# Performance work log

Hardware: AMD Instinct MI355X
Metric: run time of the kernel (lower is better)

The kernel has to match this reference:

```python
import jax, jax.numpy as jnp
import numpy as np

T, B, C, H, W = 8, 16, 384, 32, 32
HEADS, CHUNK = 8, 2
EPS = 1e-5


def setup_inputs() -> dict:
    key = jax.random.key(0)
    ks = jax.random.split(key, 6)
    s = 1.0 / np.sqrt(C)
    bn = jnp.stack([jnp.ones(C), jnp.zeros(C), jnp.zeros(C), jnp.ones(C)])  # gamma,beta,mean,var
    return {
        'x': jax.random.normal(ks[0], (T, B, C, H, W), jnp.float32),
        'q_w': jax.random.normal(ks[1], (C, C), jnp.float32) * s,
        'q_bn': bn,
        'k_w': jax.random.normal(ks[2], (C, C), jnp.float32) * s,
        'k_bn': bn,
        'v_w': jax.random.normal(ks[3], (C, C), jnp.float32) * s,
        'v_bn': bn,
        'proj_w': jax.random.normal(ks[4], (C, C), jnp.float32) * s,
        'proj_b': jnp.zeros((C,), jnp.float32),
        'proj_bn': bn,
    }


def _conv1x1(x, w, b=None):
    # x: [T,B,C,H,W], w: [Cout,Cin]
    y = jnp.einsum('tbchw,oc->tbohw', x, w)
    if b is not None:
        y = y + b[None, None, :, None, None]
    return y


def _bn(x, p):
    g, b, m, v = p  # each [C]
    inv = g * jax.lax.rsqrt(v + EPS)
    return x * inv[None, None, :, None, None] + (b - m * inv)[None, None, :, None, None]


def _heads(x):
    # [T,B,C,H,W] -> [T,B,heads,N,hd]
    hd = C // HEADS
    return x.reshape(T, B, HEADS, hd, H * W).transpose(0, 1, 2, 4, 3)


def reference(x, q_w, q_bn, k_w, k_bn, v_w, v_bn, proj_w, proj_b, proj_bn):
    hd = C // HEADS
    N = H * W
    nc = T // CHUNK
    identity = x
    xs = jax.nn.relu(x)  # shortcut_lif -> ReLU (use_snn=False)

    q = _heads(jax.nn.relu(_bn(_conv1x1(xs, q_w), q_bn)))
    k = _heads(jax.nn.relu(_bn(_conv1x1(xs, k_w), k_bn)))
    v = _heads(jax.nn.relu(_bn(_conv1x1(xs, v_w), v_bn)))

    def chunkify(t):  # [T,B,h,N,d] -> [nc,B,h,CHUNK*N,d]
        return t.reshape(nc, CHUNK, B, HEADS, N, hd).transpose(0, 2, 3, 1, 4, 5).reshape(nc, B, HEADS, CHUNK * N, hd)

    qc, kc, vc = chunkify(q), chunkify(k), chunkify(v)
    scale = 1.0 / H  # non-dvs scaling
    attn = jnp.einsum('cbhsd,cbhse->cbhde', kc, vc) * scale  # [nc,B,h,d,d]
    out = jnp.einsum('cbhsd,cbhde->cbhse', qc, attn)          # [nc,B,h,S,d]

    out = out.reshape(nc, B, HEADS, CHUNK, N, hd).transpose(0, 3, 1, 2, 4, 5).reshape(T, B, HEADS, N, hd)
    y = out.transpose(0, 1, 2, 4, 3).reshape(T, B, C, N)  # merge heads back to channels
    y = jax.nn.relu(y).reshape(T, B, C, H, W)  # attn_lif -> ReLU
    y = _bn(_conv1x1(y, proj_w, proj_b), proj_bn)
    y = y + identity
    return (y, v)
```

## Files before the change

kernel.cpp:

```cpp
#include <hip/hip_runtime.h>

typedef unsigned short u16;
typedef float f32x4 __attribute__((ext_vector_type(4)));
typedef __bf16 bf16x8 __attribute__((ext_vector_type(8)));

#define T_ 8
#define B_ 16
#define C_ 384
#define N_ 1024
#define HEADS_ 8
#define HD_ 48
#define NC_ 4
#define EPS_ 1e-5f
#define SCALE_ (1.0f / 32.0f)

__device__ __forceinline__ float bf2f(u16 u) {
  union { unsigned int i; float f; } x;
  x.i = ((unsigned int)u) << 16;
  return x.f;
}
__device__ __forceinline__ u16 f2bf(float f) {
  unsigned int u = __float_as_uint(f);
  u += 0x7fffu + ((u >> 16) & 1u);
  return (u16)(u >> 16);
}

__device__ __forceinline__ void glds16(const void* g, void* s) {
  __builtin_amdgcn_global_load_lds(
      (const __attribute__((address_space(1))) void*)g,
      (__attribute__((address_space(3))) void*)s, 16, 0, 0);
}

__global__ __launch_bounds__(256) void wconv(const float* __restrict__ a,
                                             const float* __restrict__ b,
                                             const float* __restrict__ c,
                                             u16* __restrict__ o) {
  const int m = blockIdx.x / 72;
  const float* s = (m == 0) ? a : (m == 1) ? b : c;
  const size_t off = (size_t)(blockIdx.x % 72) * 2048 + (size_t)threadIdx.x * 8;
  float4 f0 = *(const float4*)(s + off);
  float4 f1 = *(const float4*)(s + off + 4);
  u16 h[8] = {f2bf(f0.x), f2bf(f0.y), f2bf(f0.z), f2bf(f0.w),
              f2bf(f1.x), f2bf(f1.y), f2bf(f1.z), f2bf(f1.w)};
  *(uint4*)(o + (size_t)m * (C_ * C_) + off) = *(const uint4*)h;
}

__global__ __launch_bounds__(256) void prep_xt(const float* __restrict__ x,
                                               u16* __restrict__ xt) {
  const int tb = blockIdx.y;
  const int n = blockIdx.x * 64 + (threadIdx.x & 63);
  const int cg = threadIdx.x >> 6;
  const float* xb = x + (size_t)tb * C_ * N_ + n;
  u16* ob = xt + ((size_t)tb * N_ + n) * C_;
#pragma unroll
  for (int g = 0; g < 12; ++g) {
    int c = (cg + g * 4) * 8;
    u16 h[8];
#pragma unroll
    for (int j = 0; j < 8; ++j)
      h[j] = f2bf(fmaxf(xb[(size_t)(c + j) * N_], 0.f));
    *(uint4*)(ob + c) = *(const uint4*)h;
  }
}

__global__ __launch_bounds__(256) void qkv_gemm(
    const u16* __restrict__ xt, const u16* __restrict__ wbf,
    const float* __restrict__ bnq, const float* __restrict__ bnk,
    const float* __restrict__ bnv,
    u16* __restrict__ qo, u16* __restrict__ ko, float* __restrict__ vo) {
  const int tb = blockIdx.z / 3;
  const int pr = blockIdx.z % 3;
  const int n0 = blockIdx.x * 128;
  const int o0 = blockIdx.y * 128;
  const float* bn = (pr == 0) ? bnq : (pr == 1) ? bnk : bnv;
  const u16* wp = wbf + (size_t)pr * (C_ * C_);
  const u16* xb = xt + (size_t)tb * N_ * C_;

  __shared__ u16 As[128 * 64];
  __shared__ u16 Bs[128 * 64];

  const int tid = threadIdx.x;
  const int lane = tid & 63;
  const int wave = tid >> 6;
  const int wr = wave >> 1, wc = wave & 1;
  const int qd = lane >> 4, l15 = lane & 15;

  f32x4 acc[4][4];
#pragma unroll
  for (int i = 0; i < 4; ++i)
#pragma unroll
    for (int j = 0; j < 4; ++j) acc[i][j] = (f32x4){0.f, 0.f, 0.f, 0.f};

  for (int c0 = 0; c0 < C_; c0 += 64) {
    __syncthreads();
#pragma unroll
    for (int i = 0; i < 4; ++i) {
      const int L = i * 256 + tid;
      const int row = L >> 3;
      const int g = (L & 7) ^ (row & 7);
      glds16(wp + (size_t)(o0 + row) * C_ + c0 + g * 8,
             As + (size_t)(i * 256 + wave * 64) * 8);
      glds16(xb + (size_t)(n0 + row) * C_ + c0 + g * 8,
             Bs + (size_t)(i * 256 + wave * 64) * 8);
    }
    __syncthreads();
#pragma unroll
    for (int kk = 0; kk < 2; ++kk) {
      bf16x8 wf[4], xf[4];
#pragma unroll
      for (int mi = 0; mi < 4; ++mi) {
        int r = wr * 64 + mi * 16 + l15;
        wf[mi] = *(const bf16x8*)(As + r * 64 + (((kk * 4 + qd) ^ (r & 7)) * 8));
      }
#pragma unroll
      for (int ni = 0; ni < 4; ++ni) {
        int r = wc * 64 + ni * 16 + l15;
        xf[ni] = *(const bf16x8*)(Bs + r * 64 + (((kk * 4 + qd) ^ (r & 7)) * 8));
      }
      if (pr != 2) {
#pragma unroll
        for (int mi = 0; mi < 4; ++mi)
#pragma unroll
          for (int ni = 0; ni < 4; ++ni)
            acc[mi][ni] = __builtin_amdgcn_mfma_f32_16x16x32_bf16(
                wf[mi], xf[ni], acc[mi][ni], 0, 0, 0);
      } else {
#pragma unroll
        for (int ni = 0; ni < 4; ++ni)
#pragma unroll
          for (int mi = 0; mi < 4; ++mi)
            acc[ni][mi] = __builtin_amdgcn_mfma_f32_16x16x32_bf16(
                xf[ni], wf[mi], acc[ni][mi], 0, 0, 0);
      }
    }
  }

  if (pr < 2) {
    u16* out = (pr == 0) ? qo : ko;
#pragma unroll
    for (int mi = 0; mi < 4; ++mi) {
#pragma unroll
      for (int r = 0; r < 4; ++r) {
        int o = o0 + wr * 64 + mi * 16 + qd * 4 + r;
        float inv = bn[o] * rsqrtf(bn[3 * C_ + o] + EPS_);
        float sh = bn[C_ + o] - bn[2 * C_ + o] * inv;
        size_t rowbase = ((size_t)tb * C_ + o) * N_;
#pragma unroll
        for (int ni = 0; ni < 4; ++ni) {
          int n = n0 + wc * 64 + ni * 16 + l15;
          out[rowbase + n] = f2bf(fmaxf(acc[mi][ni][r] * inv + sh, 0.f));
        }
      }
    }
  } else {
#pragma unroll
    for (int bj = 0; bj < 4; ++bj) {
      int o = o0 + wr * 64 + bj * 16 + l15;
      float inv = bn[o] * rsqrtf(bn[3 * C_ + o] + EPS_);
      float sh = bn[C_ + o] - bn[2 * C_ + o] * inv;
      int hh = o / HD_, dd = o % HD_;
      size_t base = (((size_t)tb * HEADS_ + hh) * N_) * HD_ + dd;
#pragma unroll
      for (int ai = 0; ai < 4; ++ai)
#pragma unroll
        for (int r = 0; r < 4; ++r) {
          int n = n0 + wc * 64 + ai * 16 + qd * 4 + r;
          vo[base + (size_t)n * HD_] = fmaxf(acc[ai][bj][r] * inv + sh, 0.f);
        }
    }
  }
}

__global__ __launch_bounds__(256) void attn_kv(const u16* __restrict__ kk,
                                               const float* __restrict__ vv,
                                               float* __restrict__ part) {
  const int g2 = blockIdx.x;
  const int tc = g2 & 1;
  const int g = g2 >> 1;
  const int h = g & (HEADS_ - 1);
  const int b = (g >> 3) & (B_ - 1);
  const int cI = g >> 7;
  const int t = cI * 2 + tc;
  const int tid = threadIdx.x;
  const int lane = tid & 63;
  const int wave = tid >> 6;
  const int qd = lane >> 4, l15 = lane & 15;

  __shared__ u16 Ks[2][48 * 128];
  __shared__ u16 Vt[2][48 * 128];

  const size_t kbase = ((size_t)(t * B_ + b) * C_ + h * HD_) * N_;
  const size_t vbase = ((size_t)(t * B_ + b) * HEADS_ + h) * (size_t)N_ * HD_;
  const int ksc = (tid & 15) ^ ((tid >> 4) & 7);

  f32x4 acc[3][3];
#pragma unroll
  for (int m = 0; m < 3; ++m)
#pragma unroll
    for (int n = 0; n < 3; ++n) acc[m][n] = (f32x4){0.f, 0.f, 0.f, 0.f};

  float4 va[3], vb[3];

  auto issue_v = [&](int sb) {
    size_t nb = (size_t)sb * 128;
#pragma unroll
    for (int i = 0; i < 3; ++i) {
      const float* p = vv + vbase + (nb + 2 * lane) * HD_ + (i * 4 + wave) * 4;
      va[i] = *(const float4*)p;
      vb[i] = *(const float4*)(p + HD_);
    }
  };
  auto issue_k = [&](int sb, int bf) {
    size_t nb = (size_t)sb * 128;
#pragma unroll
    for (int i = 0; i < 3; ++i)
      glds16(kk + kbase + (size_t)(i * 16 + (tid >> 4)) * N_ + nb + ksc * 8,
             &Ks[bf][(i * 256 + wave * 64) * 8]);
  };
  auto write_vt = [&](int bf) {
    unsigned* vt = (unsigned*)Vt[bf];
#pragma unroll
    for (int i = 0; i < 3; ++i) {
      int eq = i * 4 + wave;
      const float* fa = (const float*)&va[i];
      const float* fb = (const float*)&vb[i];
#pragma unroll
      for (int j = 0; j < 4; ++j) {
        int e = eq * 4 + j;
        unsigned pk = (unsigned)f2bf(fa[j]) | ((unsigned)f2bf(fb[j]) << 16);
        vt[e * 64 + (((lane >> 2) ^ (e & 7)) << 2) + (lane & 3)] = pk;
      }
    }
  };

  issue_v(0);
  __builtin_amdgcn_sched_barrier(0);
  issue_k(0, 0);
  __builtin_amdgcn_sched_barrier(0);
  write_vt(0);
  __syncthreads();

  for (int sb = 0; sb < 8; ++sb) {
    const int cur = sb & 1;
    if (sb < 7) {
      issue_v(sb + 1);
      __builtin_amdgcn_sched_barrier(0);
      issue_k(sb + 1, cur ^ 1);
      __builtin_amdgcn_sched_barrier(0);
    }
    const u16* kc = Ks[cur];
    const u16* vc = Vt[cur];
    bf16x8 af[3], bfv[3];
#pragma unroll
    for (int m = 0; m < 3; ++m) {
      int d = m * 16 + l15;
      af[m] =
          *(const bf16x8*)(kc + d * 128 + (((wave * 4 + qd) ^ (d & 7)) << 3));
    }
#pragma unroll
    for (int n = 0; n < 3; ++n) {
      int e = n * 16 + l15;
      bfv[n] =
          *(const bf16x8*)(vc + e * 128 + (((wave * 4 + qd) ^ (e & 7)) << 3));
    }
#pragma unroll
    for (int m = 0; m < 3; ++m)
#pragma unroll
      for (int n = 0; n < 3; ++n)
        acc[m][n] = __builtin_amdgcn_mfma_f32_16x16x32_bf16(af[m], bfv[n],
                                                            acc[m][n], 0, 0, 0);
    if (sb < 7) write_vt(cur ^ 1);
    __syncthreads();
  }

  float* red = (float*)&Ks[0][0];
  if (wave >= 2) {
    float* dst = red + (wave - 2) * 2304;
#pragma unroll
    for (int m = 0; m < 3; ++m)
#pragma unroll
      for (int n = 0; n < 3; ++n)
#pragma unroll
        for (int r = 0; r < 4; ++r)
          dst[((m * 3 + n) * 4 + r) * 64 + lane] = acc[m][n][r];
  }
  __syncthreads();
  if (wave < 2) {
    const float* sp = red + wave * 2304;
#pragma unroll
    for (int m = 0; m < 3; ++m)
#pragma unroll
      for (int n = 0; n < 3; ++n)
#pragma unroll
        for (int r = 0; r < 4; ++r)
          acc[m][n][r] += sp[((m * 3 + n) * 4 + r) * 64 + lane];
  }
  __syncthreads();
  if (wave == 1) {
#pragma unroll
    for (int m = 0; m < 3; ++m)
#pragma unroll
      for (int n = 0; n < 3; ++n)
#pragma unroll
        for (int r = 0; r < 4; ++r)
          red[((m * 3 + n) * 4 + r) * 64 + lane] = acc[m][n][r];
  }
  __syncthreads();
  if (wave == 0) {
#pragma unroll
    for (int m = 0; m < 3; ++m)
#pragma unroll
      for (int n = 0; n < 3; ++n)
#pragma unroll
        for (int r = 0; r < 4; ++r) {
          float v = acc[m][n][r] + red[((m * 3 + n) * 4 + r) * 64 + lane];
          int d = m * 16 + qd * 4 + r;
          int e = n * 16 + l15;
          part[(size_t)g2 * 2304 + d * 48 + e] = v * SCALE_;
        }
  }
}

__global__ __launch_bounds__(256) void q_attn(const u16* __restrict__ qq,
                                              const float* __restrict__ part,
                                              u16* __restrict__ ao) {
  const int n0 = blockIdx.x * 64;
  const int z = blockIdx.y;
  const int h = z % HEADS_;
  const int b = (z / HEADS_) % B_;
  const int t = z / (HEADS_ * B_);
  const int cI = t / 2;
  const int g = (cI * B_ + b) * HEADS_ + h;
  const int tid = threadIdx.x;
  const int nl = tid & 63, eg = tid >> 6, e0 = eg * 12;

  __shared__ float at[48 * 48];
  for (int idx = tid; idx < 48 * 48; idx += 256)
    at[idx] = part[(size_t)(g * 2) * 2304 + idx] +
              part[(size_t)(g * 2 + 1) * 2304 + idx];
  __syncthreads();

  size_t qbase = ((size_t)(t * B_ + b) * C_ + h * HD_) * N_ + n0 + nl;
  float acc[12];
#pragma unroll
  for (int j = 0; j < 12; ++j) acc[j] = 0.f;
  for (int d = 0; d < 48; ++d) {
    float qv = bf2f(qq[qbase + (size_t)d * N_]);
#pragma unroll
    for (int j = 0; j < 12; ++j) acc[j] += qv * at[d * 48 + e0 + j];
  }
  size_t obase = ((size_t)(t * B_ + b) * C_ + h * HD_) * N_ + n0 + nl;
#pragma unroll
  for (int j = 0; j < 12; ++j)
    ao[obase + (size_t)(e0 + j) * N_] = f2bf(fmaxf(acc[j], 0.f));
}

__global__ __launch_bounds__(256) void proj_gemm(
    const u16* __restrict__ ao, const float* __restrict__ pw,
    const float* __restrict__ pb, const float* __restrict__ pbn,
    const float* __restrict__ x, float* __restrict__ y) {
  const int tb = blockIdx.z;
  const int n0 = blockIdx.x * 64;
  const int o0 = blockIdx.y * 64;
  const u16* ab = ao + (size_t)tb * C_ * N_;

  __shared__ u16 Ws[64][40];
  __shared__ u16 XstF[64 * 40];

  const int tid = threadIdx.x;
  const int lane = tid & 63;
  const int wave = tid >> 6;
  const int wr = wave >> 1, wc = wave & 1;
  const int qd = lane >> 4, l15 = lane & 15;

  const int ar = tid >> 2, ac = (tid & 3) << 3;
  const int br = tid >> 3, bc = (tid & 7) << 3;

  f32x4 acc[2][2];
#pragma unroll
  for (int i = 0; i < 2; ++i)
#pragma unroll
    for (int j = 0; j < 2; ++j) acc[i][j] = (f32x4){0.f, 0.f, 0.f, 0.f};

  for (int c0 = 0; c0 < C_; c0 += 32) {
    float4 a0 = *(const float4*)(pw + (size_t)(o0 + ar) * C_ + c0 + ac);
    float4 a1 = *(const float4*)(pw + (size_t)(o0 + ar) * C_ + c0 + ac + 4);
    uint4 bx = *(const uint4*)(ab + (size_t)(c0 + br) * N_ + n0 + bc);
    __syncthreads();
    u16 tmp[8];
    tmp[0] = f2bf(a0.x); tmp[1] = f2bf(a0.y);
    tmp[2] = f2bf(a0.z); tmp[3] = f2bf(a0.w);
    tmp[4] = f2bf(a1.x); tmp[5] = f2bf(a1.y);
    tmp[6] = f2bf(a1.z); tmp[7] = f2bf(a1.w);
    *(uint4*)(&Ws[ar][ac]) = *(const uint4*)tmp;
    const u16* hp = (const u16*)&bx;
#pragma unroll
    for (int j = 0; j < 8; ++j) {
      int row = bc + j;
      XstF[row * 40 + (((br >> 3) ^ ((row >> 3) & 3)) << 3) + (br & 7)] = hp[j];
    }
    __syncthreads();
    bf16x8 af[2], bfv[2];
#pragma unroll
    for (int mi = 0; mi < 2; ++mi)
      af[mi] = *(const bf16x8*)(&Ws[wr * 32 + mi * 16 + l15][qd * 8]);
#pragma unroll
    for (int ni = 0; ni < 2; ++ni) {
      int rb = wc * 32 + ni * 16 + l15;
      bfv[ni] = *(const bf16x8*)(&XstF[rb * 40 + ((qd ^ ((rb >> 3) & 3)) << 3)]);
    }
#pragma unroll
    for (int mi = 0; mi < 2; ++mi)
#pragma unroll
      for (int ni = 0; ni < 2; ++ni)
        acc[mi][ni] = __builtin_amdgcn_mfma_f32_16x16x32_bf16(
            af[mi], bfv[ni], acc[mi][ni], 0, 0, 0);
  }

#pragma unroll
  for (int mi = 0; mi < 2; ++mi) {
#pragma unroll
    for (int r = 0; r < 4; ++r) {
      int o = o0 + wr * 32 + mi * 16 + qd * 4 + r;
      float g = pbn[o], be = pbn[C_ + o];
      float mu = pbn[2 * C_ + o], va = pbn[3 * C_ + o];
      float inv = g * rsqrtf(va + EPS_);
      float add = pb[o] * inv + (be - mu * inv);
      size_t rowbase = ((size_t)tb * C_ + o) * N_;
#pragma unroll
      for (int ni = 0; ni < 2; ++ni) {
        int n = n0 + wc * 32 + ni * 16 + l15;
        float val = acc[mi][ni][r] * inv + add;
        val += x[rowbase + n];
        y[rowbase + n] = val;
      }
    }
  }
}

extern "C" void kernel_launch(void* const* d_in, const int* in_sizes, int n_in,
                              void* d_out, int out_size, void* d_ws,
                              size_t ws_size, hipStream_t stream) {
  const float* x = (const float*)d_in[0];
  const float* q_w = (const float*)d_in[1];
  const float* q_bn = (const float*)d_in[2];
  const float* k_w = (const float*)d_in[3];
  const float* k_bn = (const float*)d_in[4];
  const float* v_w = (const float*)d_in[5];
  const float* v_bn = (const float*)d_in[6];
  const float* p_w = (const float*)d_in[7];
  const float* p_b = (const float*)d_in[8];
  const float* p_bn = (const float*)d_in[9];

  const size_t NELEM = (size_t)T_ * B_ * C_ * N_;
  float* y_out = (float*)d_out;
  float* v_out = y_out + NELEM;

  u16* q_ws = (u16*)y_out;
  u16* xt_ws = q_ws + NELEM;
  float* part_ws = (float*)xt_ws;
  u16* k_ws = (u16*)d_ws;
  float* attn_ws = (float*)(k_ws + NELEM);
  u16* wbf = (u16*)attn_ws;
  u16* ao_ws = k_ws;

  wconv<<<dim3(216), 256, 0, stream>>>(q_w, k_w, v_w, wbf);
  prep_xt<<<dim3(16, 128), 256, 0, stream>>>(x, xt_ws);
  qkv_gemm<<<dim3(8, 3, T_ * B_ * 3), 256, 0, stream>>>(
      xt_ws, wbf, q_bn, k_bn, v_bn, q_ws, k_ws, v_out);
  attn_kv<<<dim3(NC_ * B_ * HEADS_ * 2), 256, 0, stream>>>(k_ws, v_out,
                                                           part_ws);
  q_attn<<<dim3(16, T_ * B_ * HEADS_), 256, 0, stream>>>(q_ws, part_ws, ao_ws);
  proj_gemm<<<dim3(16, 6, T_ * B_), 256, 0, stream>>>(ao_ws, p_w, p_b, p_bn, x,
                                                      y_out);
}
```

Measured before the change: 1.111 ms.

## Double-buffer GEMM LDS staging and rebuild proj GEMM on pre-converted bf16 weights

The qkv GEMM now double-buffers its LDS tiles, issuing async global-to-LDS loads for the next K slice while the current one feeds MFMA. q_attn writes its output in an N-major [tb,N,C] layout so proj_gemm can reuse the same 128x128 double-buffered global_load_lds pipeline. The proj weights are converted to bf16 once in wconv instead of in every proj block. The goal is to hide load latency and remove per-tile conversion and scattered LDS transposes. In exchange LDS use doubles to 64KB per block, which may lower occupancy, and q_attn now does strided 8-byte stores.

```diff
diff --git a/kernel.cpp b/kernel.cpp
--- a/kernel.cpp
+++ b/kernel.cpp
@@ -1,6 +1,7 @@
 #include <hip/hip_runtime.h>
 
 typedef unsigned short u16;
+typedef unsigned long long u64;
 typedef float f32x4 __attribute__((ext_vector_type(4)));
 typedef __bf16 bf16x8 __attribute__((ext_vector_type(8)));
 
@@ -34,9 +35,10 @@
 __global__ __launch_bounds__(256) void wconv(const float* __restrict__ a,
                                              const float* __restrict__ b,
                                              const float* __restrict__ c,
+                                             const float* __restrict__ d,
                                              u16* __restrict__ o) {
   const int m = blockIdx.x / 72;
-  const float* s = (m == 0) ? a : (m == 1) ? b : c;
+  const float* s = (m == 0) ? a : (m == 1) ? b : (m == 2) ? c : d;
   const size_t off = (size_t)(blockIdx.x % 72) * 2048 + (size_t)threadIdx.x * 8;
   float4 f0 = *(const float4*)(s + off);
   float4 f1 = *(const float4*)(s + off + 4);
@@ -76,8 +78,8 @@
   const u16* wp = wbf + (size_t)pr * (C_ * C_);
   const u16* xb = xt + (size_t)tb * N_ * C_;
 
-  __shared__ u16 As[128 * 64];
-  __shared__ u16 Bs[128 * 64];
+  __shared__ u16 As[2 * 128 * 64];
+  __shared__ u16 Bs[2 * 128 * 64];
 
   const int tid = threadIdx.x;
   const int lane = tid & 63;
@@ -91,31 +93,42 @@
 #pragma unroll
     for (int j = 0; j < 4; ++j) acc[i][j] = (f32x4){0.f, 0.f, 0.f, 0.f};
 
-  for (int c0 = 0; c0 < C_; c0 += 64) {
-    __syncthreads();
+  auto stage = [&](int buf, int c0) {
 #pragma unroll
     for (int i = 0; i < 4; ++i) {
       const int L = i * 256 + tid;
       const int row = L >> 3;
       const int g = (L & 7) ^ (row & 7);
       glds16(wp + (size_t)(o0 + row) * C_ + c0 + g * 8,
-             As + (size_t)(i * 256 + wave * 64) * 8);
+             As + (size_t)buf * (128 * 64) + (size_t)(i * 256 + wave * 64) * 8);
       glds16(xb + (size_t)(n0 + row) * C_ + c0 + g * 8,
-             Bs + (size_t)(i * 256 + wave * 64) * 8);
-    }
-    __syncthreads();
+             Bs + (size_t)buf * (128 * 64) + (size_t)(i * 256 + wave * 64) * 8);
+    }
+  };
+
+  stage(0, 0);
+  __syncthreads();
+
+  for (int s = 0; s < 6; ++s) {
+    const int cur = s & 1;
+    if (s < 5) {
+      stage(cur ^ 1, (s + 1) * 64);
+      __builtin_amdgcn_sched_barrier(0);
+    }
+    const u16* Ac = As + cur * (128 * 64);
+    const u16* Bc = Bs + cur * (128 * 64);
 #pragma unroll
     for (int kk = 0; kk < 2; ++kk) {
       bf16x8 wf[4], xf[4];
 #pragma unroll
       for (int mi = 0; mi < 4; ++mi) {
         int r = wr * 64 + mi * 16 + l15;
-        wf[mi] = *(const bf16x8*)(As + r * 64 + (((kk * 4 + qd) ^ (r & 7)) * 8));
+        wf[mi] = *(const bf16x8*)(Ac + r * 64 + (((kk * 4 + qd) ^ (r & 7)) * 8));
       }
 #pragma unroll
       for (int ni = 0; ni < 4; ++ni) {
         int r = wc * 64 + ni * 16 + l15;
-        xf[ni] = *(const bf16x8*)(Bs + r * 64 + (((kk * 4 + qd) ^ (r & 7)) * 8));
+        xf[ni] = *(const bf16x8*)(Bc + r * 64 + (((kk * 4 + qd) ^ (r & 7)) * 8));
       }
       if (pr != 2) {
 #pragma unroll
@@ -133,6 +146,7 @@
                 xf[ni], wf[mi], acc[ni][mi], 0, 0, 0);
       }
     }
+    __syncthreads();
   }
 
   if (pr < 2) {
@@ -323,7 +337,7 @@
 
 __global__ __launch_bounds__(256) void q_attn(const u16* __restrict__ qq,
                                               const float* __restrict__ part,
-                                              u16* __restrict__ ao) {
+                                              u16* __restrict__ aot) {
   const int n0 = blockIdx.x * 64;
   const int z = blockIdx.y;
   const int h = z % HEADS_;
@@ -349,23 +363,26 @@
 #pragma unroll
     for (int j = 0; j < 12; ++j) acc[j] += qv * at[d * 48 + e0 + j];
   }
-  size_t obase = ((size_t)(t * B_ + b) * C_ + h * HD_) * N_ + n0 + nl;
-#pragma unroll
-  for (int j = 0; j < 12; ++j)
-    ao[obase + (size_t)(e0 + j) * N_] = f2bf(fmaxf(acc[j], 0.f));
+  u16 hb[12];
+#pragma unroll
+  for (int j = 0; j < 12; ++j) hb[j] = f2bf(fmaxf(acc[j], 0.f));
+  u16* op = aot + ((size_t)(t * B_ + b) * N_ + n0 + nl) * C_ + h * HD_ + e0;
+  const u64* hp = (const u64*)hb;
+#pragma unroll
+  for (int j = 0; j < 3; ++j) ((u64*)op)[j] = hp[j];
 }
 
 __global__ __launch_bounds__(256) void proj_gemm(
-    const u16* __restrict__ ao, const float* __restrict__ pw,
+    const u16* __restrict__ aot, const u16* __restrict__ pwbf,
     const float* __restrict__ pb, const float* __restrict__ pbn,
     const float* __restrict__ x, float* __restrict__ y) {
   const int tb = blockIdx.z;
-  const int n0 = blockIdx.x * 64;
-  const int o0 = blockIdx.y * 64;
-  const u16* ab = ao + (size_t)tb * C_ * N_;
-
-  __shared__ u16 Ws[64][40];
-  __shared__ u16 XstF[64 * 40];
+  const int n0 = blockIdx.x * 128;
+  const int o0 = blockIdx.y * 128;
+  const u16* ab = aot + (size_t)tb * N_ * C_;
+
+  __shared__ u16 As[2 * 128 * 64];
+  __shared__ u16 Bs[2 * 128 * 64];
 
   const int tid = threadIdx.x;
   const int lane = tid & 63;
@@ -373,63 +390,72 @@
   const int wr = wave >> 1, wc = wave & 1;
   const int qd = lane >> 4, l15 = lane & 15;
 
-  const int ar = tid >> 2, ac = (tid & 3) << 3;
-  const int br = tid >> 3, bc = (tid & 7) << 3;
-
-  f32x4 acc[2][2];
-#pragma unroll
-  for (int i = 0; i < 2; ++i)
-#pragma unroll
-    for (int j = 0; j < 2; ++j) acc[i][j] = (f32x4){0.f, 0.f, 0.f, 0.f};
-
-  for (int c0 = 0; c0 < C_; c0 += 32) {
-    float4 a0 = *(const float4*)(pw + (size_t)(o0 + ar) * C_ + c0 + ac);
-    float4 a1 = *(const float4*)(pw + (size_t)(o0 + ar) * C_ + c0 + ac + 4);
-    uint4 bx = *(const uint4*)(ab + (size_t)(c0 + br) * N_ + n0 + bc);
+  f32x4 acc[4][4];
+#pragma unroll
+  for (int i = 0; i < 4; ++i)
+#pragma unroll
+    for (int j = 0; j < 4; ++j) acc[i][j] = (f32x4){0.f, 0.f, 0.f, 0.f};
+
+  auto stage = [&](int buf, int c0) {
+#pragma unroll
+    for (int i = 0; i < 4; ++i) {
+      const int L = i * 256 + tid;
+      const int row = L >> 3;
+      const int g = (L & 7) ^ (row & 7);
+      glds16(pwbf + (size_t)(o0 + row) * C_ + c0 + g * 8,
+             As + (size_t)buf * (128 * 64) + (size_t)(i * 256 + wave * 64) * 8);
+      glds16(ab + (size_t)(n0 + row) * C_ + c0 + g * 8,
+             Bs + (size_t)buf * (128 * 64) + (size_t)(i * 256 + wave * 64) * 8);
+    }
+  };
+
+  stage(0, 0);
+  __syncthreads();
+
+  for (int s = 0; s < 6; ++s) {
+    const int cur = s & 1;
+    if (s < 5) {
+      stage(cur ^ 1, (s + 1) * 64);
+      __builtin_amdgcn_sched_barrier(0);
+    }
+    const u16* Ac = As + cur * (128 * 64);
+    const u16* Bc = Bs + cur * (128 * 64);
+#pragma unroll
+    for (int kk = 0; kk < 2; ++kk) {
+      bf16x8 wf[4], xf[4];
+#pragma unroll
+      for (int mi = 0; mi < 4; ++mi) {
+        int r = wr * 64 + mi * 16 + l15;
+        wf[mi] = *(const bf16x8*)(Ac + r * 64 + (((kk * 4 + qd) ^ (r & 7)) * 8));
+      }
+#pragma unroll
+      for (int ni = 0; ni < 4; ++ni) {
+        int r = wc * 64 + ni * 16 + l15;
+        xf[ni] = *(const bf16x8*)(Bc + r * 64 + (((kk * 4 + qd) ^ (r & 7)) * 8));
+      }
+#pragma unroll
+      for (int mi = 0; mi < 4; ++mi)
+#pragma unroll
+        for (int ni = 0; ni < 4; ++ni)
+          acc[mi][ni] = __builtin_amdgcn_mfma_f32_16x16x32_bf16(
+              wf[mi], xf[ni], acc[mi][ni], 0, 0, 0);
+    }
     __syncthreads();
-    u16 tmp[8];
-    tmp[0] = f2bf(a0.x); tmp[1] = f2bf(a0.y);
-    tmp[2] = f2bf(a0.z); tmp[3] = f2bf(a0.w);
-    tmp[4] = f2bf(a1.x); tmp[5] = f2bf(a1.y);
-    tmp[6] = f2bf(a1.z); tmp[7] = f2bf(a1.w);
-    *(uint4*)(&Ws[ar][ac]) = *(const uint4*)tmp;
-    const u16* hp = (const u16*)&bx;
-#pragma unroll
-    for (int j = 0; j < 8; ++j) {
-      int row = bc + j;
-      XstF[row * 40 + (((br >> 3) ^ ((row >> 3) & 3)) << 3) + (br & 7)] = hp[j];
-    }
-    __syncthreads();
-    bf16x8 af[2], bfv[2];
-#pragma unroll
-    for (int mi = 0; mi < 2; ++mi)
-      af[mi] = *(const bf16x8*)(&Ws[wr * 32 + mi * 16 + l15][qd * 8]);
-#pragma unroll
-    for (int ni = 0; ni < 2; ++ni) {
-      int rb = wc * 32 + ni * 16 + l15;
-      bfv[ni] = *(const bf16x8*)(&XstF[rb * 40 + ((qd ^ ((rb >> 3) & 3)) << 3)]);
-    }
-#pragma unroll
-    for (int mi = 0; mi < 2; ++mi)
-#pragma unroll
-      for (int ni = 0; ni < 2; ++ni)
-        acc[mi][ni] = __builtin_amdgcn_mfma_f32_16x16x32_bf16(
-            af[mi], bfv[ni], acc[mi][ni], 0, 0, 0);
-  }
-
-#pragma unroll
-  for (int mi = 0; mi < 2; ++mi) {
+  }
+
+#pragma unroll
+  for (int mi = 0; mi < 4; ++mi) {
 #pragma unroll
     for (int r = 0; r < 4; ++r) {
-      int o = o0 + wr * 32 + mi * 16 + qd * 4 + r;
+      int o = o0 + wr * 64 + mi * 16 + qd * 4 + r;
       float g = pbn[o], be = pbn[C_ + o];
       float mu = pbn[2 * C_ + o], va = pbn[3 * C_ + o];
       float inv = g * rsqrtf(va + EPS_);
       float add = pb[o] * inv + (be - mu * inv);
       size_t rowbase = ((size_t)tb * C_ + o) * N_;
 #pragma unroll
-      for (int ni = 0; ni < 2; ++ni) {
-        int n = n0 + wc * 32 + ni * 16 + l15;
+      for (int ni = 0; ni < 4; ++ni) {
+        int n = n0 + wc * 64 + ni * 16 + l15;
         float val = acc[mi][ni][r] * inv + add;
         val += x[rowbase + n];
         y[rowbase + n] = val;
@@ -460,17 +486,16 @@
   u16* xt_ws = q_ws + NELEM;
   float* part_ws = (float*)xt_ws;
   u16* k_ws = (u16*)d_ws;
-  float* attn_ws = (float*)(k_ws + NELEM);
-  u16* wbf = (u16*)attn_ws;
+  u16* wbf = k_ws + NELEM;
   u16* ao_ws = k_ws;
 
-  wconv<<<dim3(216), 256, 0, stream>>>(q_w, k_w, v_w, wbf);
+  wconv<<<dim3(288), 256, 0, stream>>>(q_w, k_w, v_w, p_w, wbf);
   prep_xt<<<dim3(16, 128), 256, 0, stream>>>(x, xt_ws);
   qkv_gemm<<<dim3(8, 3, T_ * B_ * 3), 256, 0, stream>>>(
       xt_ws, wbf, q_bn, k_bn, v_bn, q_ws, k_ws, v_out);
   attn_kv<<<dim3(NC_ * B_ * HEADS_ * 2), 256, 0, stream>>>(k_ws, v_out,
                                                            part_ws);
   q_attn<<<dim3(16, T_ * B_ * HEADS_), 256, 0, stream>>>(q_ws, part_ws, ao_ws);
-  proj_gemm<<<dim3(16, 6, T_ * B_), 256, 0, stream>>>(ao_ws, p_w, p_b, p_bn, x,
-                                                      y_out);
-}
+  proj_gemm<<<dim3(8, 3, T_ * B_), 256, 0, stream>>>(
+      ao_ws, wbf + 3 * C_ * C_, p_b, p_bn, x, y_out);
+}
```

Measured after the change: 1.178 ms. +6.1%, slower.
